# Kernel optimization log

Measured on AMD Instinct MI355X. Metric: run time of the kernel, lower is better.

The kernel has to match this reference:

```python
import jax, jax.numpy as jnp
import numpy as np

B, N, D_IN, D_OUT = 4, 1024, 128, 64
SLOPE = 0.01  # LeakyReLU negative slope


def leaky_relu(x):
    return jnp.where(x >= 0, x, SLOPE * x)


def setup_inputs() -> dict:
    key = jax.random.key(0)
    k_x, k_m, k_w1, k_w2, k_a, k_l = jax.random.split(key, 6)
    x = jax.random.normal(k_x, (B, N, D_IN), dtype=jnp.float32)
    # binary adjacency mask; add self-loops so every row has >=1 neighbor
    mask = jax.random.bernoulli(k_m, 0.05, (B, N, N)).astype(jnp.float32)
    eye = jnp.eye(N, dtype=jnp.float32)[None]
    A_shape = jnp.maximum(mask, eye)
    w1 = jax.random.normal(k_w1, (D_IN, D_OUT), dtype=jnp.float32)
    w2 = jax.random.normal(k_w2, (D_IN, D_OUT), dtype=jnp.float32)
    a = jax.random.normal(k_a, (D_OUT,), dtype=jnp.float32)
    lin_w = jax.random.normal(k_l, (D_OUT, D_IN), dtype=jnp.float32) * (1.0 / np.sqrt(D_IN))
    return {"x": x, "A_shape": A_shape, "w1": w1, "w2": w2, "a": a, "lin_w": lin_w}


def reference(x, A_shape, w1, w2, a, lin_w):
    # x: [B,N,D_in], A_shape: [B,N,N] mask
    x1 = x @ w1            # [B,N,D_out]  (dst features)
    x2 = x @ w2            # [B,N,D_out]  (src features)
    # GATv2 additive score: leakyrelu(x1_i + x2_j) . a -> [B,N,N]
    S = leaky_relu(x1[:, :, None, :] + x2[:, None, :, :])
    S = jnp.einsum('bijd,d->bij', S, a)
    S = jnp.tanh(S / 8.0) * 8.0
    A = jnp.exp(S) * A_shape
    A = A / jnp.sum(A, axis=-1, keepdims=True)
    out = A @ x            # [B,N,D_in] weighted aggregate of raw features
    out = out @ lin_w.T    # [B,N,D_out]
    return leaky_relu(out)
```

## Files before the change

kernel.cpp:

```cpp
#include <hip/hip_runtime.h>
#include <math.h>

#define BB 4
#define NN 1024
#define DIN 128
#define DOUT 64
#define SLOPE 0.01f
#define CAP 256


__global__ __launch_bounds__(64, 8) void proj_kernel(
    const float* __restrict__ x, const float* __restrict__ w1,
    const float* __restrict__ w2, const float* __restrict__ lin_w,
    float* __restrict__ x12, float* __restrict__ lwP) {
  int l = threadIdx.x;
  if (blockIdx.x >= BB * NN) {
    int base = (blockIdx.x - BB * NN) * 1024;
#pragma unroll
    for (int i = 0; i < 16; ++i) {
      int idx = base + i * 64 + l;
      int k2 = idx >> 7;
      int rem = idx & 127;
      int d = rem >> 1, r = rem & 1;
      lwP[idx] = lin_w[d * DIN + 2 * k2 + r];
    }
    return;
  }
  int row = blockIdx.x;
  __shared__ __align__(16) float xl[DIN];
  reinterpret_cast<float2*>(xl)[l] =
      reinterpret_cast<const float2*>(x + (size_t)row * DIN)[l];
  __syncthreads();
  const float* w1c = w1 + l;
  const float* w2c = w2 + l;
  float a1 = 0.f, a2 = 0.f;
#pragma unroll 8
  for (int k = 0; k < DIN; ++k) {
    float xv = xl[k];
    a1 = fmaf(xv, w1c[k * DOUT], a1);
    a2 = fmaf(xv, w2c[k * DOUT], a2);
  }
  x12[(size_t)row * 128 + l] = a1;
  x12[(size_t)row * 128 + DOUT + l] = a2;
}

__device__ __forceinline__ float fast_edge_exp(float sc) {
  float z = sc * 0.125f;
  z = fminf(10.f, fmaxf(-10.f, z));
  float u = __expf(2.f * z);
  float th = (u - 1.f) / (u + 1.f);
  return __expf(8.f * th);
}

__global__ __launch_bounds__(128, 8) void gat_row_kernel(
    const float* __restrict__ x, const float* __restrict__ A_shape,
    const float* __restrict__ a_vec, const float* __restrict__ lwP,
    const float* __restrict__ x12, float* __restrict__ out) {
  int tid = threadIdx.x;
  int w = tid >> 6;
  int lane = tid & 63;
  int bi = blockIdx.x * 2 + w;
  int b = bi >> 10;

  __shared__ int eidx_s[2][CAP];
  __shared__ __align__(16) float agg_s[2][DIN];
  int* eidx = eidx_s[w];
  float* aggw = agg_s[w];

  const float* mask_row = A_shape + (size_t)bi * NN;
  float mv[16];
#pragma unroll
  for (int c = 0; c < 16; ++c) mv[c] = mask_row[c * 64 + lane];
  int base = 0;
#pragma unroll
  for (int c = 0; c < 16; ++c) {
    bool pred = (mv[c] != 0.f);
    unsigned long long m = __ballot(pred);
    int prefix = __popcll(m & ((1ull << lane) - 1ull));
    int slot = base + prefix;
    if (pred && slot < CAP) eidx[slot] = c * 64 + lane;
    base += __popcll(m);
  }
  int nz = base < CAP ? base : CAP;

  int l16 = lane & 15;
  int grp = lane >> 4;
  float4 x1v = *reinterpret_cast<const float4*>(x12 + (size_t)bi * 128 + l16 * 4);
  float4 avv = *reinterpret_cast<const float4*>(a_vec + l16 * 4);
  const float* x2b = x12 + (size_t)b * NN * 128 + DOUT;
  const float* xb = x + (size_t)b * NN * DIN;
  float acc[8] = {0.f, 0.f, 0.f, 0.f, 0.f, 0.f, 0.f, 0.f};
  float esum = 0.f;
  for (int s = 0; s < nz; s += 4) {
    int sg = s + grp;
    bool valid = sg < nz;
    int j = eidx[valid ? sg : nz - 1];
    const float* x2r = x2b + (size_t)j * 128;
    const float* xr = xb + (size_t)j * DIN;
    float4 x2v = *reinterpret_cast<const float4*>(x2r + l16 * 4);
    float4 xa = *reinterpret_cast<const float4*>(xr + l16 * 8);
    float4 xc = *reinterpret_cast<const float4*>(xr + l16 * 8 + 4);
    float z, sc = 0.f;
    z = x1v.x + x2v.x; sc = fmaf(z >= 0.f ? z : SLOPE * z, avv.x, sc);
    z = x1v.y + x2v.y; sc = fmaf(z >= 0.f ? z : SLOPE * z, avv.y, sc);
    z = x1v.z + x2v.z; sc = fmaf(z >= 0.f ? z : SLOPE * z, avv.z, sc);
    z = x1v.w + x2v.w; sc = fmaf(z >= 0.f ? z : SLOPE * z, avv.w, sc);
    sc += __shfl_xor(sc, 1, 64);
    sc += __shfl_xor(sc, 2, 64);
    sc += __shfl_xor(sc, 4, 64);
    sc += __shfl_xor(sc, 8, 64);
    float e = valid ? fast_edge_exp(sc) : 0.f;
    esum += e;
    acc[0] = fmaf(e, xa.x, acc[0]);
    acc[1] = fmaf(e, xa.y, acc[1]);
    acc[2] = fmaf(e, xa.z, acc[2]);
    acc[3] = fmaf(e, xa.w, acc[3]);
    acc[4] = fmaf(e, xc.x, acc[4]);
    acc[5] = fmaf(e, xc.y, acc[5]);
    acc[6] = fmaf(e, xc.z, acc[6]);
    acc[7] = fmaf(e, xc.w, acc[7]);
  }
  esum += __shfl_xor(esum, 16, 64);
  esum += __shfl_xor(esum, 32, 64);
  float inv = 1.f / esum;
#pragma unroll
  for (int r = 0; r < 8; ++r) {
    acc[r] += __shfl_xor(acc[r], 16, 64);
    acc[r] += __shfl_xor(acc[r], 32, 64);
    acc[r] *= inv;
  }
  if (grp == 0) {
    float4 lo = {acc[0], acc[1], acc[2], acc[3]};
    float4 hi = {acc[4], acc[5], acc[6], acc[7]};
    *reinterpret_cast<float4*>(aggw + l16 * 8) = lo;
    *reinterpret_cast<float4*>(aggw + l16 * 8 + 4) = hi;
  }
  __builtin_amdgcn_wave_barrier();

  float o = 0.f;
#pragma unroll 8
  for (int k2 = 0; k2 < 64; ++k2) {
    float2 ag = *reinterpret_cast<const float2*>(aggw + k2 * 2);
    float2 lw = *reinterpret_cast<const float2*>(lwP + k2 * 128 + lane * 2);
    o = fmaf(ag.y, lw.y, fmaf(ag.x, lw.x, o));
  }
  o = o >= 0.f ? o : SLOPE * o;
  out[(size_t)bi * DOUT + lane] = o;
}

extern "C" void kernel_launch(void* const* d_in, const int* in_sizes, int n_in,
                              void* d_out, int out_size, void* d_ws, size_t ws_size,
                              hipStream_t stream) {
  const float* x = (const float*)d_in[0];
  const float* A_shape = (const float*)d_in[1];
  const float* w1 = (const float*)d_in[2];
  const float* w2 = (const float*)d_in[3];
  const float* a = (const float*)d_in[4];
  const float* lin_w = (const float*)d_in[5];
  float* out = (float*)d_out;
  float* x12 = (float*)d_ws;
  float* lwP = (float*)d_ws + (size_t)BB * NN * 128;

  proj_kernel<<<BB * NN + 8, 64, 0, stream>>>(x, w1, w2, lin_w, x12, lwP);
  gat_row_kernel<<<BB * NN / 2, 128, 0, stream>>>(x, A_shape, a, lwP, x12, out);
}
```

Measured before the change: 101.7 us.

## Fuse projection and GAT row kernels into one cooperative kernel with grid sync

Merges the projection kernel into the attention kernel and launches it cooperatively. Each wave computes its own row's x1 into shared memory and x2 into a compact global buffer, then a grid-wide sync separates this from the neighbor aggregation. This removes one kernel launch and the x1 global round trip. The mask is now read with float4 loads. A grid sync across 2048 blocks needs them all resident at once (launch bounds changed to 4 blocks per CU), so the launch may fail or the barrier may cost more than the launch it saves.

```diff
diff --git a/kernel.cpp b/kernel.cpp
--- a/kernel.cpp
+++ b/kernel.cpp
@@ -1,5 +1,8 @@
 #include <hip/hip_runtime.h>
+#include <hip/hip_cooperative_groups.h>
 #include <math.h>
+
+namespace cg = cooperative_groups;
 
 #define BB 4
 #define NN 1024
@@ -9,41 +12,6 @@
 #define CAP 256
 
 
-__global__ __launch_bounds__(64, 8) void proj_kernel(
-    const float* __restrict__ x, const float* __restrict__ w1,
-    const float* __restrict__ w2, const float* __restrict__ lin_w,
-    float* __restrict__ x12, float* __restrict__ lwP) {
-  int l = threadIdx.x;
-  if (blockIdx.x >= BB * NN) {
-    int base = (blockIdx.x - BB * NN) * 1024;
-#pragma unroll
-    for (int i = 0; i < 16; ++i) {
-      int idx = base + i * 64 + l;
-      int k2 = idx >> 7;
-      int rem = idx & 127;
-      int d = rem >> 1, r = rem & 1;
-      lwP[idx] = lin_w[d * DIN + 2 * k2 + r];
-    }
-    return;
-  }
-  int row = blockIdx.x;
-  __shared__ __align__(16) float xl[DIN];
-  reinterpret_cast<float2*>(xl)[l] =
-      reinterpret_cast<const float2*>(x + (size_t)row * DIN)[l];
-  __syncthreads();
-  const float* w1c = w1 + l;
-  const float* w2c = w2 + l;
-  float a1 = 0.f, a2 = 0.f;
-#pragma unroll 8
-  for (int k = 0; k < DIN; ++k) {
-    float xv = xl[k];
-    a1 = fmaf(xv, w1c[k * DOUT], a1);
-    a2 = fmaf(xv, w2c[k * DOUT], a2);
-  }
-  x12[(size_t)row * 128 + l] = a1;
-  x12[(size_t)row * 128 + DOUT + l] = a2;
-}
-
 __device__ __forceinline__ float fast_edge_exp(float sc) {
   float z = sc * 0.125f;
   z = fminf(10.f, fmaxf(-10.f, z));
@@ -52,42 +20,79 @@
   return __expf(8.f * th);
 }
 
-__global__ __launch_bounds__(128, 8) void gat_row_kernel(
+__global__ __launch_bounds__(128, 4) void gat_fused_kernel(
     const float* __restrict__ x, const float* __restrict__ A_shape,
-    const float* __restrict__ a_vec, const float* __restrict__ lwP,
-    const float* __restrict__ x12, float* __restrict__ out) {
+    const float* __restrict__ a_vec, const float* __restrict__ w1,
+    const float* __restrict__ w2, const float* __restrict__ lin_w,
+    float* __restrict__ x2g, float* __restrict__ lwP,
+    float* __restrict__ out) {
   int tid = threadIdx.x;
   int w = tid >> 6;
   int lane = tid & 63;
   int bi = blockIdx.x * 2 + w;
   int b = bi >> 10;
 
+  __shared__ __align__(16) float xl[2][DIN];
+  __shared__ __align__(16) float x1s[2][DOUT];
   __shared__ int eidx_s[2][CAP];
   __shared__ __align__(16) float agg_s[2][DIN];
+  float* xlw = xl[w];
+  float* x1w = x1s[w];
   int* eidx = eidx_s[w];
   float* aggw = agg_s[w];
 
-  const float* mask_row = A_shape + (size_t)bi * NN;
-  float mv[16];
+  reinterpret_cast<float2*>(xlw)[lane] =
+      reinterpret_cast<const float2*>(x + (size_t)bi * DIN)[lane];
+  __syncthreads();
+  {
+    const float* w1c = w1 + lane;
+    const float* w2c = w2 + lane;
+    float a1 = 0.f, a2 = 0.f;
+#pragma unroll 8
+    for (int k = 0; k < DIN; ++k) {
+      float xv = xlw[k];
+      a1 = fmaf(xv, w1c[k * DOUT], a1);
+      a2 = fmaf(xv, w2c[k * DOUT], a2);
+    }
+    x1w[lane] = a1;
+    x2g[(size_t)bi * DOUT + lane] = a2;
+  }
+  if (blockIdx.x < 64) {
+    int idx = blockIdx.x * 128 + tid;
+    int k2 = idx >> 7;
+    int rem = idx & 127;
+    int d = rem >> 1, r = rem & 1;
+    lwP[idx] = lin_w[d * DIN + 2 * k2 + r];
+  }
+
+  cg::this_grid().sync();
+
+  const float4* mrow4 =
+      reinterpret_cast<const float4*>(A_shape + (size_t)bi * NN);
+  float mvf[16];
 #pragma unroll
-  for (int c = 0; c < 16; ++c) mv[c] = mask_row[c * 64 + lane];
+  for (int c = 0; c < 4; ++c)
+    *reinterpret_cast<float4*>(&mvf[c * 4]) = mrow4[c * 64 + lane];
   int base = 0;
 #pragma unroll
-  for (int c = 0; c < 16; ++c) {
-    bool pred = (mv[c] != 0.f);
-    unsigned long long m = __ballot(pred);
-    int prefix = __popcll(m & ((1ull << lane) - 1ull));
-    int slot = base + prefix;
-    if (pred && slot < CAP) eidx[slot] = c * 64 + lane;
-    base += __popcll(m);
+  for (int c = 0; c < 4; ++c) {
+#pragma unroll
+    for (int q = 0; q < 4; ++q) {
+      bool pred = (mvf[c * 4 + q] != 0.f);
+      unsigned long long m = __ballot(pred);
+      int prefix = __popcll(m & ((1ull << lane) - 1ull));
+      int slot = base + prefix;
+      if (pred && slot < CAP) eidx[slot] = c * 256 + lane * 4 + q;
+      base += __popcll(m);
+    }
   }
   int nz = base < CAP ? base : CAP;
 
   int l16 = lane & 15;
   int grp = lane >> 4;
-  float4 x1v = *reinterpret_cast<const float4*>(x12 + (size_t)bi * 128 + l16 * 4);
+  float4 x1v = *reinterpret_cast<const float4*>(x1w + l16 * 4);
   float4 avv = *reinterpret_cast<const float4*>(a_vec + l16 * 4);
-  const float* x2b = x12 + (size_t)b * NN * 128 + DOUT;
+  const float* x2b = x2g + (size_t)b * NN * DOUT;
   const float* xb = x + (size_t)b * NN * DIN;
   float acc[8] = {0.f, 0.f, 0.f, 0.f, 0.f, 0.f, 0.f, 0.f};
   float esum = 0.f;
@@ -95,11 +100,9 @@
     int sg = s + grp;
     bool valid = sg < nz;
     int j = eidx[valid ? sg : nz - 1];
-    const float* x2r = x2b + (size_t)j * 128;
-    const float* xr = xb + (size_t)j * DIN;
-    float4 x2v = *reinterpret_cast<const float4*>(x2r + l16 * 4);
-    float4 xa = *reinterpret_cast<const float4*>(xr + l16 * 8);
-    float4 xc = *reinterpret_cast<const float4*>(xr + l16 * 8 + 4);
+    float4 x2v = *reinterpret_cast<const float4*>(x2b + (size_t)j * DOUT + l16 * 4);
+    float4 xa = *reinterpret_cast<const float4*>(xb + (size_t)j * DIN + l16 * 8);
+    float4 xc = *reinterpret_cast<const float4*>(xb + (size_t)j * DIN + l16 * 8 + 4);
     float z, sc = 0.f;
     z = x1v.x + x2v.x; sc = fmaf(z >= 0.f ? z : SLOPE * z, avv.x, sc);
     z = x1v.y + x2v.y; sc = fmaf(z >= 0.f ? z : SLOPE * z, avv.y, sc);
@@ -158,9 +161,12 @@
   const float* a = (const float*)d_in[4];
   const float* lin_w = (const float*)d_in[5];
   float* out = (float*)d_out;
-  float* x12 = (float*)d_ws;
-  float* lwP = (float*)d_ws + (size_t)BB * NN * 128;
+  float* x2g = (float*)d_ws;
+  float* lwP = (float*)d_ws + (size_t)BB * NN * DOUT;
 
-  proj_kernel<<<BB * NN + 8, 64, 0, stream>>>(x, w1, w2, lin_w, x12, lwP);
-  gat_row_kernel<<<BB * NN / 2, 128, 0, stream>>>(x, A_shape, a, lwP, x12, out);
+  void* args[] = {(void*)&x, (void*)&A_shape, (void*)&a,   (void*)&w1,
+                  (void*)&w2, (void*)&lin_w,  (void*)&x2g, (void*)&lwP,
+                  (void*)&out};
+  hipLaunchCooperativeKernel((const void*)gat_fused_kernel,
+                             dim3(BB * NN / 2), dim3(128), args, 0, stream);
 }
```

Result: slower. 286.5 us (+181.7%).
